# Kernel tuning notes

Hardware: AMD Instinct MI355X
Metric: run time of the kernel (lower is better)

Reference implementation:

```python
import jax, jax.numpy as jnp
import numpy as np

B, C_IN, C_OUT, RED, H, W = 8, 256, 64, 16, 256, 256
K = 3


def setup_inputs() -> dict:
    key = jax.random.key(0)
    k1, k2, k3, k4, k5 = jax.random.split(key, 5)
    x = jax.random.normal(k1, (B, C_OUT, H, W), dtype=jnp.float32)
    vec = jax.random.normal(k2, (B, C_IN), dtype=jnp.float32)
    # ChanNorm affine params
    g = jnp.ones((1, C_OUT, 1, 1), dtype=jnp.float32)
    b = jnp.zeros((1, C_OUT, 1, 1), dtype=jnp.float32)
    # conv_du MLP (torch Linear weights: [out, in], no bias)
    w1 = jax.random.normal(k3, (C_IN // RED, C_IN), dtype=jnp.float32) / np.sqrt(C_IN)
    w2 = jax.random.normal(k4, (C_OUT, C_IN // RED), dtype=jnp.float32) / np.sqrt(C_IN // RED)
    # Conv2DMod weight, kaiming normal fan_in (leaky_relu a=0): std=sqrt(2/fan_in)
    fan_in = C_OUT * K * K
    wconv = jax.random.normal(k5, (C_OUT, C_OUT, K, K), dtype=jnp.float32) * np.sqrt(2.0 / fan_in)
    return {"x": x, "vec": vec, "g": g, "b": b, "w1": w1, "w2": w2, "wconv": wconv}


def reference(x, vec, g, b, w1, w2, wconv):
    eps_norm = 1e-5
    eps_mod = 1e-8
    # ChanNorm: normalize over channel dim (unbiased=False var)
    mean = jnp.mean(x, axis=1, keepdims=True)
    var = jnp.mean((x - mean) ** 2, axis=1, keepdims=True)
    nx = (x - mean) / jnp.sqrt(var + eps_norm) * g + b
    # style MLP: Linear -> LeakyReLU(0.1) -> Linear (no biases)
    hid = jax.nn.leaky_relu(vec @ w1.T, negative_slope=0.1)
    sty = hid @ w2.T  # [B, C_OUT]
    # per-sample modulated weights: [B, O, I, K, K]
    weights = wconv[None, :, :, :, :] * (sty[:, None, :, None, None] + 1.0)
    # demodulate
    d = jax.lax.rsqrt(jnp.sum(weights ** 2, axis=(2, 3, 4), keepdims=True) + eps_mod)
    weights = weights * d
    # grouped conv with groups=B == per-sample conv; same padding for k=3,s=1,d=1 -> 1
    pad = ((H - 1) * 0 + 1 * (K - 1)) // 2
    def per_sample_conv(xi, wi):
        # xi: [C,H,W], wi: [O,I,K,K]
        return jax.lax.conv_general_dilated(
            xi[None], wi, window_strides=(1, 1),
            padding=[(pad, pad), (pad, pad)],
            dimension_numbers=("NCHW", "OIHW", "NCHW"))[0]
    out = jax.vmap(per_sample_conv)(nx, weights)  # [B, O, H, W]
    return out + x
```

## Files before the change

### kernel.cpp

```cpp
#include <hip/hip_runtime.h>
#include <hip/hip_bf16.h>

typedef __hip_bfloat16 bf16;
typedef __attribute__((ext_vector_type(8))) short short8;
typedef __attribute__((ext_vector_type(4))) float float4v;

#define Hd 256
#define Wd 256
#define HW 65536
#define CO 64

__global__ __launch_bounds__(64) void k1_style(
    const float* __restrict__ vec, const float* __restrict__ w1,
    const float* __restrict__ w2, const float* __restrict__ wconv,
    bf16* __restrict__ wA)
{
    int o = blockIdx.x;
    int s = blockIdx.y;
    int i = threadIdx.x;

    float sv[4];
#pragma unroll
    for (int q = 0; q < 4; ++q) sv[q] = vec[s * 256 + q * 64 + i];

    float hid[16];
#pragma unroll
    for (int j = 0; j < 16; ++j) {
        float p = 0.f;
#pragma unroll
        for (int q = 0; q < 4; ++q) p += sv[q] * w1[j * 256 + q * 64 + i];
#pragma unroll
        for (int off = 32; off >= 1; off >>= 1) p += __shfl_xor(p, off, 64);
        hid[j] = p > 0.f ? p : 0.1f * p;
    }
    float sty = 0.f;
#pragma unroll
    for (int j = 0; j < 16; ++j) sty += w2[i * 16 + j] * hid[j];
    float msty = sty + 1.0f;

    float wrow[9];
#pragma unroll
    for (int tt = 0; tt < 9; ++tt) wrow[tt] = wconv[(o * 64 + i) * 9 + tt] * msty;
    float ss = 0.f;
#pragma unroll
    for (int tt = 0; tt < 9; ++tt) ss += wrow[tt] * wrow[tt];
#pragma unroll
    for (int off = 32; off >= 1; off >>= 1) ss += __shfl_xor(ss, off, 64);
    float d = rsqrtf(ss + 1e-8f);

    bf16* wAs = wA + s * (18 * 64 * 32);
#pragma unroll
    for (int tt = 0; tt < 9; ++tt) {
        int k = tt * 64 + i;
        wAs[(k >> 5) * 2048 + o * 32 + (k & 31)] = (bf16)(wrow[tt] * d);
    }
}

#define PXB 32
#define ROWS 8
#define TR 10
#define WL 34
#define ROW_ELEMS (8 * WL * 8)

__global__ __launch_bounds__(256, 2) void k3_fused(
    const float* __restrict__ x, const float* __restrict__ gg,
    const float* __restrict__ bb, const bf16* __restrict__ wA,
    float* __restrict__ out)
{
    int w0 = blockIdx.x * PXB;
    int h0 = blockIdx.y * ROWS;
    int s  = blockIdx.z;
    int t  = threadIdx.x;
    __shared__ __align__(16) bf16 tile[TR * ROW_ELEMS];
    __shared__ float sg[64], sb[64];
    __shared__ float2 sbi[64];
    __shared__ float2 sms[TR * WL];
    if (t < 64) {
        float gv = gg[t];
        sg[t] = gv; sb[t] = bb[t];
        sbi[t] = make_float2(bb[t], 1.0f / gv);
    }
    __syncthreads();

    for (int p = t; p < TR * WL; p += 256) {
        int dr = p / WL, wl = p - dr * WL;
        int grow = h0 + dr - 1, wabs = w0 + wl - 1;
        bf16* dst = &tile[dr * ROW_ELEMS + wl * 8];
        if (grow >= 0 && grow < Hd && wabs >= 0 && wabs < Wd) {
            const float* xp = x + (size_t)s * (CO * HW) + (size_t)grow * Wd + wabs;
            float v[64], s1 = 0.f, s2 = 0.f;
#pragma unroll
            for (int c = 0; c < 64; ++c) {
                float f = xp[(size_t)c * HW];
                v[c] = f; s1 += f; s2 += f * f;
            }
            float mean = s1 * (1.f / 64);
            float var  = s2 * (1.f / 64) - mean * mean;
            float rstd = rsqrtf(var + 1e-5f);
            sms[p] = make_float2(mean, sqrtf(var + 1e-5f));
#pragma unroll
            for (int c8 = 0; c8 < 8; ++c8) {
                bf16 ov[8];
#pragma unroll
                for (int k = 0; k < 8; ++k) {
                    int c = c8 * 8 + k;
                    ov[k] = (bf16)((v[c] - mean) * rstd * sg[c] + sb[c]);
                }
                *(uint4*)&dst[c8 * (WL * 8)] = *(uint4*)ov;
            }
        } else {
            sms[p] = make_float2(0.f, 0.f);
            uint4 z = make_uint4(0u, 0u, 0u, 0u);
#pragma unroll
            for (int c8 = 0; c8 < 8; ++c8) *(uint4*)&dst[c8 * (WL * 8)] = z;
        }
    }
    __syncthreads();

    int wave = t >> 6, lane = t & 63;
    int mi = wave & 1, ni = wave >> 1;
    int col = lane & 15, quad = lane >> 4;

    const bf16* wAs = wA + s * (18 * 64 * 32);
    short8 afrag[18][2];
#pragma unroll
    for (int kc = 0; kc < 18; ++kc)
#pragma unroll
        for (int mt = 0; mt < 2; ++mt) {
            union { uint4 u; short8 s8; } a;
            a.u = *(const uint4*)&wAs[kc * 2048 + (mi * 32 + mt * 16 + col) * 32 + quad * 8];
            afrag[kc][mt] = a.s8;
        }

    int wl_i = ni * 16 + col + 1;

#pragma unroll 2
    for (int r = 0; r < ROWS; ++r) {
        float4v acc[2];
        acc[0] = (float4v)0.f; acc[1] = (float4v)0.f;
#pragma unroll
        for (int kc = 0; kc < 18; ++kc) {
            int tap = kc >> 1;
            int kh = tap / 3, kw = tap - kh * 3;
            int ch8 = (kc & 1) * 4 + quad;
            int wl = ni * 16 + col + kw;
            union { uint4 u; short8 s8; } b;
            b.u = *(const uint4*)&tile[(r + kh) * ROW_ELEMS + (ch8 * WL + wl) * 8];
            acc[0] = __builtin_amdgcn_mfma_f32_16x16x32_bf16(afrag[kc][0], b.s8, acc[0], 0, 0, 0);
            acc[1] = __builtin_amdgcn_mfma_f32_16x16x32_bf16(afrag[kc][1], b.s8, acc[1], 0, 0, 0);
        }
        int grow = h0 + r;
        int wpx  = w0 + ni * 16 + col;
        float2 ms = sms[(r + 1) * WL + wl_i];
#pragma unroll
        for (int mt = 0; mt < 2; ++mt) {
#pragma unroll
            for (int rr = 0; rr < 4; ++rr) {
                int o = mi * 32 + mt * 16 + quad * 4 + rr;
                float nxf = __bfloat162float(
                    tile[(r + 1) * ROW_ELEMS + ((o >> 3) * WL + wl_i) * 8 + (o & 7)]);
                float2 bi = sbi[o];
                float xrec = (nxf - bi.x) * bi.y * ms.y + ms.x;
                size_t idx = (size_t)(s * CO + o) * HW + (size_t)grow * Wd + wpx;
                out[idx] = acc[mt][rr] + xrec;
            }
        }
    }
}

extern "C" void kernel_launch(void* const* d_in, const int* in_sizes, int n_in,
                              void* d_out, int out_size, void* d_ws, size_t ws_size,
                              hipStream_t stream)
{
    const float* x     = (const float*)d_in[0];
    const float* vec   = (const float*)d_in[1];
    const float* g     = (const float*)d_in[2];
    const float* bb    = (const float*)d_in[3];
    const float* w1    = (const float*)d_in[4];
    const float* w2    = (const float*)d_in[5];
    const float* wconv = (const float*)d_in[6];
    float* out = (float*)d_out;

    bf16* wA = (bf16*)d_ws;

    k1_style<<<dim3(64, 8), 64, 0, stream>>>(vec, w1, w2, wconv, wA);
    k3_fused<<<dim3(8, 32, 8), 256, 0, stream>>>(x, g, bb, wA, out);
}
```

Baseline: 307.9 us.

## Halve row tile, stream weight fragments, and re-read x to cut registers

The fused conv kernel now handles 4 output rows per block instead of 8, which doubles the grid and raises launch bounds to 4 blocks per CU. Weight A-fragments are no longer held in 36 registers; they are loaded per tap and reused across the 4 rows, with all 8 accumulators kept live. The normalization pass re-reads x from global (cache) instead of buffering 64 values per thread, so registers drop enough for the higher occupancy target. The cost is a larger halo share (6 tile rows per 4 output rows, against 10 per 8), a second read of x per channel, and weight loads repeated in every block.

```diff
diff --git a/kernel.cpp b/kernel.cpp
--- a/kernel.cpp
+++ b/kernel.cpp
@@ -57,12 +57,12 @@
 }
 
 #define PXB 32
-#define ROWS 8
-#define TR 10
+#define ROWS 4
+#define TR 6
 #define WL 34
 #define ROW_ELEMS (8 * WL * 8)
 
-__global__ __launch_bounds__(256, 2) void k3_fused(
+__global__ __launch_bounds__(256, 4) void k3_fused(
     const float* __restrict__ x, const float* __restrict__ gg,
     const float* __restrict__ bb, const bf16* __restrict__ wA,
     float* __restrict__ out)
@@ -82,34 +82,36 @@
     }
     __syncthreads();
 
-    for (int p = t; p < TR * WL; p += 256) {
-        int dr = p / WL, wl = p - dr * WL;
+    if (t < TR * WL) {
+        int dr = t / WL, wl = t - dr * WL;
         int grow = h0 + dr - 1, wabs = w0 + wl - 1;
         bf16* dst = &tile[dr * ROW_ELEMS + wl * 8];
         if (grow >= 0 && grow < Hd && wabs >= 0 && wabs < Wd) {
             const float* xp = x + (size_t)s * (CO * HW) + (size_t)grow * Wd + wabs;
-            float v[64], s1 = 0.f, s2 = 0.f;
+            float s1 = 0.f, s2 = 0.f;
 #pragma unroll
             for (int c = 0; c < 64; ++c) {
                 float f = xp[(size_t)c * HW];
-                v[c] = f; s1 += f; s2 += f * f;
+                s1 += f; s2 += f * f;
             }
             float mean = s1 * (1.f / 64);
             float var  = s2 * (1.f / 64) - mean * mean;
             float rstd = rsqrtf(var + 1e-5f);
-            sms[p] = make_float2(mean, sqrtf(var + 1e-5f));
+            sms[t] = make_float2(mean, sqrtf(var + 1e-5f));
+            asm volatile("" ::: "memory");
 #pragma unroll
             for (int c8 = 0; c8 < 8; ++c8) {
                 bf16 ov[8];
 #pragma unroll
                 for (int k = 0; k < 8; ++k) {
                     int c = c8 * 8 + k;
-                    ov[k] = (bf16)((v[c] - mean) * rstd * sg[c] + sb[c]);
+                    float f = xp[(size_t)c * HW];
+                    ov[k] = (bf16)((f - mean) * rstd * sg[c] + sb[c]);
                 }
                 *(uint4*)&dst[c8 * (WL * 8)] = *(uint4*)ov;
             }
         } else {
-            sms[p] = make_float2(0.f, 0.f);
+            sms[t] = make_float2(0.f, 0.f);
             uint4 z = make_uint4(0u, 0u, 0u, 0u);
 #pragma unroll
             for (int c8 = 0; c8 < 8; ++c8) *(uint4*)&dst[c8 * (WL * 8)] = z;
@@ -122,35 +124,41 @@
     int col = lane & 15, quad = lane >> 4;
 
     const bf16* wAs = wA + s * (18 * 64 * 32);
-    short8 afrag[18][2];
+
+    float4v acc[2][4];
 #pragma unroll
-    for (int kc = 0; kc < 18; ++kc)
+    for (int mt = 0; mt < 2; ++mt)
 #pragma unroll
-        for (int mt = 0; mt < 2; ++mt) {
-            union { uint4 u; short8 s8; } a;
-            a.u = *(const uint4*)&wAs[kc * 2048 + (mi * 32 + mt * 16 + col) * 32 + quad * 8];
-            afrag[kc][mt] = a.s8;
+        for (int r = 0; r < 4; ++r) acc[mt][r] = (float4v)0.f;
+
+#pragma unroll 1
+    for (int kh = 0; kh < 3; ++kh) {
+#pragma unroll
+        for (int kw = 0; kw < 3; ++kw) {
+#pragma unroll
+            for (int half = 0; half < 2; ++half) {
+                int kc = (kh * 3 + kw) * 2 + half;
+                union { uint4 u; short8 s8; } a0, a1;
+                a0.u = *(const uint4*)&wAs[kc * 2048 + (mi * 32 + col) * 32 + quad * 8];
+                a1.u = *(const uint4*)&wAs[kc * 2048 + (mi * 32 + 16 + col) * 32 + quad * 8];
+                int ch8 = half * 4 + quad;
+#pragma unroll
+                for (int r = 0; r < 4; ++r) {
+                    union { uint4 u; short8 s8; } b;
+                    b.u = *(const uint4*)&tile[(r + kh) * ROW_ELEMS
+                                               + (ch8 * WL + ni * 16 + col + kw) * 8];
+                    acc[0][r] = __builtin_amdgcn_mfma_f32_16x16x32_bf16(a0.s8, b.s8, acc[0][r], 0, 0, 0);
+                    acc[1][r] = __builtin_amdgcn_mfma_f32_16x16x32_bf16(a1.s8, b.s8, acc[1][r], 0, 0, 0);
+                }
+            }
         }
+    }
 
+    int wpx  = w0 + ni * 16 + col;
     int wl_i = ni * 16 + col + 1;
-
-#pragma unroll 2
-    for (int r = 0; r < ROWS; ++r) {
-        float4v acc[2];
-        acc[0] = (float4v)0.f; acc[1] = (float4v)0.f;
 #pragma unroll
-        for (int kc = 0; kc < 18; ++kc) {
-            int tap = kc >> 1;
-            int kh = tap / 3, kw = tap - kh * 3;
-            int ch8 = (kc & 1) * 4 + quad;
-            int wl = ni * 16 + col + kw;
-            union { uint4 u; short8 s8; } b;
-            b.u = *(const uint4*)&tile[(r + kh) * ROW_ELEMS + (ch8 * WL + wl) * 8];
-            acc[0] = __builtin_amdgcn_mfma_f32_16x16x32_bf16(afrag[kc][0], b.s8, acc[0], 0, 0, 0);
-            acc[1] = __builtin_amdgcn_mfma_f32_16x16x32_bf16(afrag[kc][1], b.s8, acc[1], 0, 0, 0);
-        }
+    for (int r = 0; r < 4; ++r) {
         int grow = h0 + r;
-        int wpx  = w0 + ni * 16 + col;
         float2 ms = sms[(r + 1) * WL + wl_i];
 #pragma unroll
         for (int mt = 0; mt < 2; ++mt) {
@@ -162,7 +170,7 @@
                 float2 bi = sbi[o];
                 float xrec = (nxf - bi.x) * bi.y * ms.y + ms.x;
                 size_t idx = (size_t)(s * CO + o) * HW + (size_t)grow * Wd + wpx;
-                out[idx] = acc[mt][rr] + xrec;
+                out[idx] = acc[mt][r][rr] + xrec;
             }
         }
     }
@@ -184,5 +192,5 @@
     bf16* wA = (bf16*)d_ws;
 
     k1_style<<<dim3(64, 8), 64, 0, stream>>>(vec, w1, w2, wconv, wA);
-    k3_fused<<<dim3(8, 32, 8), 256, 0, stream>>>(x, g, bb, wA, out);
+    k3_fused<<<dim3(8, 64, 8), 256, 0, stream>>>(x, g, bb, wA, out);
 }
```

After: 362.9 us. +17.9%, slower.

## Split channel norm into separate pass writing NHWC bf16 intermediate

Applied to the files above, without the earlier changes.

Moves the channel normalization out of the fused conv kernel into a new kernel that reads x coalesced with float4 loads and writes a bf16 NHWC normalized tensor plus per-pixel mean/std to workspace. The conv kernel then loads halo tiles as contiguous 16-byte chunks instead of recomputing the normalization, including on halo pixels, with strided per-channel fp32 loads. In exchange it adds an extra global round trip of about 64 MB of bf16 plus the stats buffer, a second kernel launch, and drops the occupancy hint of 2 blocks per SM.

```diff
diff --git a/kernel.cpp b/kernel.cpp
--- a/kernel.cpp
+++ b/kernel.cpp
@@ -56,66 +56,119 @@
     }
 }
 
+__global__ __launch_bounds__(256) void k2_norm(
+    const float* __restrict__ x, const float* __restrict__ gg,
+    const float* __restrict__ bb, bf16* __restrict__ nx,
+    float2* __restrict__ sms)
+{
+    int h = blockIdx.x, s = blockIdx.y;
+    int t = threadIdx.x;
+    int cg = t & 15;
+    int pg = t >> 4;
+    float4 g4 = *(const float4*)&gg[cg * 4];
+    float4 b4 = *(const float4*)&bb[cg * 4];
+    const float* xrow = x + (size_t)s * ((size_t)CO * HW) + (size_t)h * Wd;
+    bf16*   nxrow  = nx  + ((size_t)s * HW + (size_t)h * Wd) * CO;
+    float2* smsrow = sms +  (size_t)s * HW + (size_t)h * Wd;
+
+#pragma unroll 1
+    for (int it = 0; it < 4; ++it) {
+        int px = it * 64 + pg * 4;
+        float4 v[4];
+#pragma unroll
+        for (int cc = 0; cc < 4; ++cc)
+            v[cc] = *(const float4*)&xrow[(size_t)(cg * 4 + cc) * HW + px];
+
+        float s1[4], s2[4];
+#pragma unroll
+        for (int pi = 0; pi < 4; ++pi) {
+            float a0 = (&v[0].x)[pi], a1 = (&v[1].x)[pi];
+            float a2 = (&v[2].x)[pi], a3 = (&v[3].x)[pi];
+            s1[pi] = (a0 + a1) + (a2 + a3);
+            s2[pi] = (a0 * a0 + a1 * a1) + (a2 * a2 + a3 * a3);
+        }
+#pragma unroll
+        for (int off = 1; off <= 8; off <<= 1)
+#pragma unroll
+            for (int pi = 0; pi < 4; ++pi) {
+                s1[pi] += __shfl_xor(s1[pi], off, 64);
+                s2[pi] += __shfl_xor(s2[pi], off, 64);
+            }
+        float mean[4], rstd[4], stdv[4];
+#pragma unroll
+        for (int pi = 0; pi < 4; ++pi) {
+            mean[pi] = s1[pi] * (1.f / 64);
+            float var = s2[pi] * (1.f / 64) - mean[pi] * mean[pi];
+            rstd[pi] = rsqrtf(var + 1e-5f);
+            stdv[pi] = sqrtf(var + 1e-5f);
+        }
+        if (cg == 0) {
+#pragma unroll
+            for (int pi = 0; pi < 4; ++pi)
+                smsrow[px + pi] = make_float2(mean[pi], stdv[pi]);
+        }
+#pragma unroll
+        for (int pi = 0; pi < 4; ++pi) {
+            union { uint2 u; bf16 hh[4]; } o;
+#pragma unroll
+            for (int cc = 0; cc < 4; ++cc) {
+                float f  = (&v[cc].x)[pi];
+                float gv = (&g4.x)[cc], bv = (&b4.x)[cc];
+                o.hh[cc] = (bf16)((f - mean[pi]) * rstd[pi] * gv + bv);
+            }
+            *(uint2*)&nxrow[(size_t)(px + pi) * CO + cg * 4] = o.u;
+        }
+    }
+}
+
 #define PXB 32
 #define ROWS 8
 #define TR 10
 #define WL 34
+#define NSITES (TR * WL)
 #define ROW_ELEMS (8 * WL * 8)
 
-__global__ __launch_bounds__(256, 2) void k3_fused(
-    const float* __restrict__ x, const float* __restrict__ gg,
-    const float* __restrict__ bb, const bf16* __restrict__ wA,
-    float* __restrict__ out)
+union U4 { uint4 u; bf16 h[8]; short8 s8; };
+
+__global__ __launch_bounds__(256) void k3_conv(
+    const bf16* __restrict__ nx, const float2* __restrict__ sms,
+    const float* __restrict__ gg, const float* __restrict__ bb,
+    const bf16* __restrict__ wA, float* __restrict__ out)
 {
     int w0 = blockIdx.x * PXB;
     int h0 = blockIdx.y * ROWS;
     int s  = blockIdx.z;
     int t  = threadIdx.x;
     __shared__ __align__(16) bf16 tile[TR * ROW_ELEMS];
-    __shared__ float sg[64], sb[64];
     __shared__ float2 sbi[64];
-    __shared__ float2 sms[TR * WL];
-    if (t < 64) {
-        float gv = gg[t];
-        sg[t] = gv; sb[t] = bb[t];
-        sbi[t] = make_float2(bb[t], 1.0f / gv);
-    }
-    __syncthreads();
-
-    for (int p = t; p < TR * WL; p += 256) {
-        int dr = p / WL, wl = p - dr * WL;
-        int grow = h0 + dr - 1, wabs = w0 + wl - 1;
-        bf16* dst = &tile[dr * ROW_ELEMS + wl * 8];
-        if (grow >= 0 && grow < Hd && wabs >= 0 && wabs < Wd) {
-            const float* xp = x + (size_t)s * (CO * HW) + (size_t)grow * Wd + wabs;
-            float v[64], s1 = 0.f, s2 = 0.f;
-#pragma unroll
-            for (int c = 0; c < 64; ++c) {
-                float f = xp[(size_t)c * HW];
-                v[c] = f; s1 += f; s2 += f * f;
-            }
-            float mean = s1 * (1.f / 64);
-            float var  = s2 * (1.f / 64) - mean * mean;
-            float rstd = rsqrtf(var + 1e-5f);
-            sms[p] = make_float2(mean, sqrtf(var + 1e-5f));
-#pragma unroll
-            for (int c8 = 0; c8 < 8; ++c8) {
-                bf16 ov[8];
-#pragma unroll
-                for (int k = 0; k < 8; ++k) {
-                    int c = c8 * 8 + k;
-                    ov[k] = (bf16)((v[c] - mean) * rstd * sg[c] + sb[c]);
-                }
-                *(uint4*)&dst[c8 * (WL * 8)] = *(uint4*)ov;
-            }
-        } else {
-            sms[p] = make_float2(0.f, 0.f);
-            uint4 z = make_uint4(0u, 0u, 0u, 0u);
-#pragma unroll
-            for (int c8 = 0; c8 < 8; ++c8) *(uint4*)&dst[c8 * (WL * 8)] = z;
-        }
-    }
-    __syncthreads();
+    if (t < 64) sbi[t] = make_float2(bb[t], 1.0f / gg[t]);
+
+    int p0 = t, p1 = t + 256;
+    bool live1 = (p1 < NSITES);
+    int dr0 = p0 / WL, wl0 = p0 - dr0 * WL;
+    int dr1 = live1 ? (p1 / WL) : 0;
+    int wl1 = live1 ? (p1 - dr1 * WL) : 0;
+    int grow0 = h0 + dr0 - 1, wab0 = w0 + wl0 - 1;
+    int grow1 = h0 + dr1 - 1, wab1 = w0 + wl1 - 1;
+    bool ok0 = (grow0 >= 0 && grow0 < Hd && wab0 >= 0 && wab0 < Wd);
+    bool ok1 = live1 && (grow1 >= 0 && grow1 < Hd && wab1 >= 0 && wab1 < Wd);
+    const bf16* np0 = nx + ((size_t)s * HW + (size_t)grow0 * Wd + wab0) * CO;
+    const bf16* np1 = nx + ((size_t)s * HW + (size_t)grow1 * Wd + wab1) * CO;
+    bf16* dst0 = &tile[dr0 * ROW_ELEMS + wl0 * 8];
+    bf16* dst1 = &tile[dr1 * ROW_ELEMS + wl1 * 8];
+    uint4 z = make_uint4(0u, 0u, 0u, 0u);
+#pragma unroll
+    for (int c8 = 0; c8 < 8; ++c8) {
+        uint4 a = ok0 ? *(const uint4*)&np0[c8 * 8] : z;
+        *(uint4*)&dst0[c8 * (WL * 8)] = a;
+    }
+    if (live1) {
+#pragma unroll
+        for (int c8 = 0; c8 < 8; ++c8) {
+            uint4 a = ok1 ? *(const uint4*)&np1[c8 * 8] : z;
+            *(uint4*)&dst1[c8 * (WL * 8)] = a;
+        }
+    }
 
     int wave = t >> 6, lane = t & 63;
     int mi = wave & 1, ni = wave >> 1;
@@ -127,13 +180,19 @@
     for (int kc = 0; kc < 18; ++kc)
 #pragma unroll
         for (int mt = 0; mt < 2; ++mt) {
-            union { uint4 u; short8 s8; } a;
+            U4 a;
             a.u = *(const uint4*)&wAs[kc * 2048 + (mi * 32 + mt * 16 + col) * 32 + quad * 8];
             afrag[kc][mt] = a.s8;
         }
+    int wpx = w0 + ni * 16 + col;
+    float2 msr[ROWS];
+#pragma unroll
+    for (int r = 0; r < ROWS; ++r)
+        msr[r] = sms[(size_t)s * HW + (size_t)(h0 + r) * Wd + wpx];
+
+    __syncthreads();
 
     int wl_i = ni * 16 + col + 1;
-
 #pragma unroll 2
     for (int r = 0; r < ROWS; ++r) {
         float4v acc[2];
@@ -143,15 +202,13 @@
             int tap = kc >> 1;
             int kh = tap / 3, kw = tap - kh * 3;
             int ch8 = (kc & 1) * 4 + quad;
-            int wl = ni * 16 + col + kw;
-            union { uint4 u; short8 s8; } b;
-            b.u = *(const uint4*)&tile[(r + kh) * ROW_ELEMS + (ch8 * WL + wl) * 8];
+            U4 b;
+            b.u = *(const uint4*)&tile[(r + kh) * ROW_ELEMS + (ch8 * WL + ni * 16 + col + kw) * 8];
             acc[0] = __builtin_amdgcn_mfma_f32_16x16x32_bf16(afrag[kc][0], b.s8, acc[0], 0, 0, 0);
             acc[1] = __builtin_amdgcn_mfma_f32_16x16x32_bf16(afrag[kc][1], b.s8, acc[1], 0, 0, 0);
         }
         int grow = h0 + r;
-        int wpx  = w0 + ni * 16 + col;
-        float2 ms = sms[(r + 1) * WL + wl_i];
+        float2 ms = msr[r];
 #pragma unroll
         for (int mt = 0; mt < 2; ++mt) {
 #pragma unroll
@@ -181,8 +238,12 @@
     const float* wconv = (const float*)d_in[6];
     float* out = (float*)d_out;
 
-    bf16* wA = (bf16*)d_ws;
+    char* wsb = (char*)d_ws;
+    bf16*   wA  = (bf16*)wsb;
+    bf16*   nx  = (bf16*)(wsb + ((size_t)1 << 20));
+    float2* sms = (float2*)(wsb + ((size_t)65 << 20));
 
     k1_style<<<dim3(64, 8), 64, 0, stream>>>(vec, w1, w2, wconv, wA);
-    k3_fused<<<dim3(8, 32, 8), 256, 0, stream>>>(x, g, bb, wA, out);
-}
+    k2_norm<<<dim3(256, 8), 256, 0, stream>>>(x, g, bb, nx, sms);
+    k3_conv<<<dim3(8, 32, 8), 256, 0, stream>>>(nx, sms, g, bb, wA, out);
+}
```

Result: slower. 320.9 us (+4.2%).
